# Optimization experiments

Hardware: AMD Instinct MI355X
Metric: run time of the kernel (lower is better)

## Reference

```python
import jax, jax.numpy as jnp
import numpy as np

_COVALENT_RADII = np.array([0.0, 0.31, 0.28, 1.28, 0.96, 0.84, 0.76, 0.71, 0.66, 0.57, 0.58, 1.66, 1.41, 1.21, 1.11, 1.07, 1.05, 1.02, 1.06, 2.03, 1.76, 1.7, 1.6, 1.53, 1.39, 1.39, 1.32, 1.26, 1.24, 1.32, 1.22, 1.18, 1.22, 1.2, 1.16, 1.19, 1.2, 2.2, 1.95, 1.9, 1.75, 1.64, 1.54, 1.47, 1.46, 1.42, 1.39, 1.45, 1.44, 1.42, 1.39, 1.39, 1.38, 1.39, 1.4, 2.44, 2.15, 2.12, 2.06, 1.98, 1.96, 1.94, 1.92, 1.92, 1.89, 1.9, 1.87, 1.87, 1.75, 1.7, 1.62, 1.51, 1.44, 1.41, 1.36, 1.36, 1.32, 1.45, 1.46, 1.48, 1.4, 1.5, 1.42, 1.38, 1.35, 1.35, 1.33, 1.35, 1.4, 1.42, 1.45, 1.5, 1.55, 1.63, 1.54], dtype=np.float32)

B = 4104      # number of molecules
NMAX = 64     # max atoms per molecule (ragged sizes in [8, 64])

def setup_inputs() -> dict:
    key = jax.random.key(0)
    num_atoms = 8 + (np.arange(B) % 57)          # deterministic ragged sizes, sum = 147744
    N = int(num_atoms.sum())
    batch_indices = np.repeat(np.arange(B), num_atoms)
    k1, k2 = jax.random.split(key)
    cart_coords = jax.random.normal(k1, (N, 3), dtype=jnp.float32) * 3.0
    species = jax.random.randint(k2, (N,), 1, 95)
    return {
        'cart_coords': cart_coords,
        'species': species.astype(jnp.int32),
        'batch_indices': jnp.asarray(batch_indices, dtype=jnp.int32),
        'num_atoms': jnp.asarray(num_atoms, dtype=jnp.int32),
        'radii_table': jnp.asarray(_COVALENT_RADII),
    }

def reference(cart_coords, species, batch_indices, num_atoms, radii_table):
    Bm = num_atoms.shape[0]
    N = cart_coords.shape[0]
    dt = cart_coords.dtype
    # within-group position of each atom (offset-based ragged indexing)
    offsets = jnp.cumsum(num_atoms) - num_atoms
    pos = jnp.arange(N) - offsets[batch_indices]
    # scatter flat ragged arrays into padded [B, NMAX, ...] layout
    padded = jnp.zeros((Bm, NMAX, 3), dt).at[batch_indices, pos].set(cart_coords)
    rpad = jnp.zeros((Bm, NMAX), dt).at[batch_indices, pos].set(radii_table[species])
    mask = jnp.arange(NMAX)[None, :] < num_atoms[:, None]          # [B, NMAX]
    # pairwise repulsion loss (same math as torch loop: diag excluded, sqrt(d2+1e-8))
    diff = padded[:, :, None, :] - padded[:, None, :, :]           # [B, NMAX, NMAX, 3]
    dist = jnp.sqrt(jnp.sum(diff * diff, axis=-1) + 1e-8)
    pair_mask = mask[:, :, None] & mask[:, None, :] & ~jnp.eye(NMAX, dtype=bool)[None]
    thr = (rpad[:, :, None] + rpad[:, None, :]) * 0.8
    pen = jnp.where(pair_mask, jax.nn.relu(thr - dist) ** 2, jnp.zeros((), dt))
    nf = jnp.maximum(num_atoms, 1).astype(dt)
    per_mol = pen.sum(axis=(1, 2)) / nf
    l_repulsion = jnp.where(num_atoms > 1, per_mol, jnp.zeros((), dt)).sum() / Bm
    # per-group mean centering (segment mean)
    mean = jax.ops.segment_sum(cart_coords, batch_indices, num_segments=Bm) / nf[:, None]
    centered = cart_coords - mean[batch_indices]
    return l_repulsion, centered
```

## Files before the change

### kernel.cpp

```cpp
#include <hip/hip_runtime.h>

#define NMAX 64
#define MPB 4

__global__ void offsets_kernel(const int* __restrict__ batch_indices, int N,
                               int* __restrict__ offsets) {
    int i = blockIdx.x * blockDim.x + threadIdx.x;
    if (i < N) {
        int b = batch_indices[i];
        if (i == 0 || batch_indices[i - 1] != b) offsets[b] = i;
    }
}

__global__ __launch_bounds__(64 * MPB) void mol_kernel(
    const float* __restrict__ coords,
    const int*   __restrict__ species,
    const int*   __restrict__ num_atoms,
    const float* __restrict__ radii,
    const int*   __restrict__ offsets,
    float* __restrict__ penv,
    float* __restrict__ out,
    int Bm) {
    const int w  = threadIdx.x >> 6;
    const int tw = threadIdx.x & 63;
    const int m  = blockIdx.x * MPB + w;

    __shared__ float4 s4[MPB][NMAX];

    int n = 0, off = 0;
    if (m < Bm) {
        n = num_atoms[m];
        off = offsets[m];
    }

    float x = 0.f, y = 0.f, z = 0.f, r = 0.f;
    if (tw < n) {
        const float* cp = coords + 3 * (size_t)(off + tw);
        x = cp[0]; y = cp[1]; z = cp[2];
        r = radii[species[off + tw]];
    }
    s4[w][tw] = make_float4(x, y, z, r);
    __syncthreads();
    if (m >= Bm || n <= 0) return;

    float sx = x, sy = y, sz = z;
    #pragma unroll
    for (int d = 32; d > 0; d >>= 1) {
        sx += __shfl_down(sx, d);
        sy += __shfl_down(sy, d);
        sz += __shfl_down(sz, d);
    }
    const float invn = 1.0f / (float)n;
    const float mx = __shfl(sx, 0) * invn;
    const float my = __shfl(sy, 0) * invn;
    const float mz = __shfl(sz, 0) * invn;

    float pen = 0.0f;
    if (tw < n) {
        #pragma unroll 4
        for (int j = 0; j < n; ++j) {
            float4 aj = s4[w][j];
            float dx = x - aj.x;
            float dy = y - aj.y;
            float dz = z - aj.z;
            float d2 = dx * dx + dy * dy + dz * dz + 1e-8f;
            float dist = sqrtf(d2);
            float thr = (r + aj.w) * 0.8f;
            float v = thr - dist;
            pen += (j != tw && v > 0.0f) ? v * v : 0.0f;
        }
    }
    #pragma unroll
    for (int d = 32; d > 0; d >>= 1) pen += __shfl_down(pen, d);
    if (tw == 0) penv[m] = (n > 1) ? pen * invn : 0.0f;

    if (tw < n) {
        float* op = out + 1 + 3 * (size_t)(off + tw);
        op[0] = x - mx;
        op[1] = y - my;
        op[2] = z - mz;
    }
}

__global__ void reduce_kernel(const float4* __restrict__ pv4, int n4,
                              const float* __restrict__ tail, int rem,
                              float* __restrict__ out, float invB) {
    __shared__ float sdata[4];
    int t = threadIdx.x;
    float s = 0.f;
    for (int i = t; i < n4; i += 256) {
        float4 v = pv4[i];
        s += v.x + v.y + v.z + v.w;
    }
    if (t < rem) s += tail[t];
    #pragma unroll
    for (int d = 32; d > 0; d >>= 1) s += __shfl_down(s, d);
    if ((t & 63) == 0) sdata[t >> 6] = s;
    __syncthreads();
    if (t == 0) out[0] = (sdata[0] + sdata[1] + sdata[2] + sdata[3]) * invB;
}

extern "C" void kernel_launch(void* const* d_in, const int* in_sizes, int n_in,
                              void* d_out, int out_size, void* d_ws, size_t ws_size,
                              hipStream_t stream) {
    const float* cart_coords   = (const float*)d_in[0];
    const int*   species       = (const int*)d_in[1];
    const int*   batch_indices = (const int*)d_in[2];
    const int*   num_atoms     = (const int*)d_in[3];
    const float* radii_table   = (const float*)d_in[4];

    const int N  = in_sizes[0] / 3;
    const int Bm = in_sizes[3];

    int*   offsets = (int*)d_ws;
    float* penv    = (float*)d_ws + Bm;
    float* out     = (float*)d_out;

    offsets_kernel<<<(N + 255) / 256, 256, 0, stream>>>(batch_indices, N, offsets);
    mol_kernel<<<(Bm + MPB - 1) / MPB, 64 * MPB, 0, stream>>>(
        cart_coords, species, num_atoms, radii_table, offsets, penv, out, Bm);

    const int n4  = Bm / 4;
    const int rem = Bm - 4 * n4;
    reduce_kernel<<<1, 256, 0, stream>>>((const float4*)penv, n4,
                                         penv + 4 * n4, rem, out, 1.0f / (float)Bm);
}
```

Baseline: 81.57 us.

## Fuse offset computation into molecule kernel and broadcast atoms via readlane

Drops the separate offsets kernel. Each wavefront now computes its molecule's start offset itself by summing num_atoms over all earlier molecules in a strided loop with a shuffle reduction. Pair coordinates are broadcast with readlane instead of being staged through shared memory, which also removes the block barrier. The cost is up to about 4K redundant num_atoms reads per wave, a quadratic total of reads over all molecules, served mostly from cache. Readlane needs a uniform lane index, and j is wave-uniform, so this is valid.

After: 87.09 us. 6.8% more time.

```diff
diff --git a/kernel.cpp b/kernel.cpp
--- a/kernel.cpp
+++ b/kernel.cpp
@@ -1,37 +1,31 @@
 #include <hip/hip_runtime.h>
 
-#define NMAX 64
 #define MPB 4
 
-__global__ void offsets_kernel(const int* __restrict__ batch_indices, int N,
-                               int* __restrict__ offsets) {
-    int i = blockIdx.x * blockDim.x + threadIdx.x;
-    if (i < N) {
-        int b = batch_indices[i];
-        if (i == 0 || batch_indices[i - 1] != b) offsets[b] = i;
-    }
+__device__ __forceinline__ float readlane_f(float v, int lane) {
+    return __builtin_bit_cast(float,
+        __builtin_amdgcn_readlane(__builtin_bit_cast(int, v), lane));
 }
 
-__global__ __launch_bounds__(64 * MPB) void mol_kernel(
+__global__ __launch_bounds__(256) void mol_kernel(
     const float* __restrict__ coords,
     const int*   __restrict__ species,
     const int*   __restrict__ num_atoms,
     const float* __restrict__ radii,
-    const int*   __restrict__ offsets,
     float* __restrict__ penv,
     float* __restrict__ out,
     int Bm) {
     const int w  = threadIdx.x >> 6;
     const int tw = threadIdx.x & 63;
     const int m  = blockIdx.x * MPB + w;
+    if (m >= Bm) return;
 
-    __shared__ float4 s4[MPB][NMAX];
-
-    int n = 0, off = 0;
-    if (m < Bm) {
-        n = num_atoms[m];
-        off = offsets[m];
-    }
+    int acc = 0;
+    for (int i = tw; i < m; i += 64) acc += num_atoms[i];
+    #pragma unroll
+    for (int d = 32; d > 0; d >>= 1) acc += __shfl_down(acc, d);
+    const int off = __shfl(acc, 0);
+    const int n   = num_atoms[m];
 
     float x = 0.f, y = 0.f, z = 0.f, r = 0.f;
     if (tw < n) {
@@ -39,9 +33,6 @@
         x = cp[0]; y = cp[1]; z = cp[2];
         r = radii[species[off + tw]];
     }
-    s4[w][tw] = make_float4(x, y, z, r);
-    __syncthreads();
-    if (m >= Bm || n <= 0) return;
 
     float sx = x, sy = y, sz = z;
     #pragma unroll
@@ -56,25 +47,23 @@
     const float mz = __shfl(sz, 0) * invn;
 
     float pen = 0.0f;
-    if (tw < n) {
-        #pragma unroll 4
-        for (int j = 0; j < n; ++j) {
-            float4 aj = s4[w][j];
-            float dx = x - aj.x;
-            float dy = y - aj.y;
-            float dz = z - aj.z;
-            float d2 = dx * dx + dy * dy + dz * dz + 1e-8f;
-            float dist = sqrtf(d2);
-            float thr = (r + aj.w) * 0.8f;
-            float v = thr - dist;
-            pen += (j != tw && v > 0.0f) ? v * v : 0.0f;
-        }
+    const bool act = (tw < n);
+    #pragma unroll 4
+    for (int j = 0; j < n; ++j) {
+        float ax = readlane_f(x, j);
+        float ay = readlane_f(y, j);
+        float az = readlane_f(z, j);
+        float ar = readlane_f(r, j);
+        float dx = x - ax, dy = y - ay, dz = z - az;
+        float dist = sqrtf(dx * dx + dy * dy + dz * dz + 1e-8f);
+        float v = (r + ar) * 0.8f - dist;
+        pen += (act && j != tw && v > 0.0f) ? v * v : 0.0f;
     }
     #pragma unroll
     for (int d = 32; d > 0; d >>= 1) pen += __shfl_down(pen, d);
     if (tw == 0) penv[m] = (n > 1) ? pen * invn : 0.0f;
 
-    if (tw < n) {
+    if (act) {
         float* op = out + 1 + 3 * (size_t)(off + tw);
         op[0] = x - mx;
         op[1] = y - my;
@@ -103,22 +92,18 @@
 extern "C" void kernel_launch(void* const* d_in, const int* in_sizes, int n_in,
                               void* d_out, int out_size, void* d_ws, size_t ws_size,
                               hipStream_t stream) {
-    const float* cart_coords   = (const float*)d_in[0];
-    const int*   species       = (const int*)d_in[1];
-    const int*   batch_indices = (const int*)d_in[2];
-    const int*   num_atoms     = (const int*)d_in[3];
-    const float* radii_table   = (const float*)d_in[4];
+    const float* cart_coords = (const float*)d_in[0];
+    const int*   species     = (const int*)d_in[1];
+    const int*   num_atoms   = (const int*)d_in[3];
+    const float* radii_table = (const float*)d_in[4];
 
-    const int N  = in_sizes[0] / 3;
     const int Bm = in_sizes[3];
 
-    int*   offsets = (int*)d_ws;
-    float* penv    = (float*)d_ws + Bm;
-    float* out     = (float*)d_out;
+    float* penv = (float*)d_ws;
+    float* out  = (float*)d_out;
 
-    offsets_kernel<<<(N + 255) / 256, 256, 0, stream>>>(batch_indices, N, offsets);
-    mol_kernel<<<(Bm + MPB - 1) / MPB, 64 * MPB, 0, stream>>>(
-        cart_coords, species, num_atoms, radii_table, offsets, penv, out, Bm);
+    mol_kernel<<<(Bm + MPB - 1) / MPB, 256, 0, stream>>>(
+        cart_coords, species, num_atoms, radii_table, penv, out, Bm);
 
     const int n4  = Bm / 4;
     const int rem = Bm - 4 * n4;
```
